# Optimization experiments

Hardware: AMD Instinct MI355X
Metric: run time of the kernel (lower is better)

## Reference

```python
import jax, jax.numpy as jnp
import numpy as np

BLOCK = 8      # block_size
HALO = 3       # halo_size
WIN = BLOCK + 2 * HALO   # 14, kv window size
NH = 8         # num_heads
DH = 32        # dim_head
DIM = 256
DIM_QK = NH * DH          # 256
DV = 256                  # dim_v = dim_out
DVH = DV // NH            # 32
SCALE = DH ** -0.5
REL = 2 * WIN - 1         # 27


def rel_logits_1d(q, rel_k, permute_mask):
    # q: (B, H, W, d); rel_k: (rel_size, d)
    B, H, W, d = q.shape
    rel_size = rel_k.shape[0]
    win = (rel_size + 1) // 2
    x = jnp.einsum('bhwd,rd->bhwr', q, rel_k).reshape(-1, W, rel_size)
    # skew trick: pad + reshape turns absolute into relative indexing
    x = jnp.pad(x, ((0, 0), (0, 0), (0, 1))).reshape(x.shape[0], -1)
    x = jnp.pad(x, ((0, 0), (0, rel_size - W))).reshape(-1, W + 1, rel_size)
    x = x[:, :W, win - 1:]
    x = jnp.broadcast_to(x.reshape(B, H, 1, W, win), (B, H, win, W, win))
    return jnp.transpose(x, permute_mask)


def pos_embed_rel(q, height_rel, width_rel):
    # q: (B*NH, num_blocks, block*block, DH)
    B, BB, HW, dh = q.shape
    q4 = q.reshape(-1, BLOCK, BLOCK, dh)
    rel_w = rel_logits_1d(q4, width_rel, (0, 1, 3, 2, 4))
    rel_h = rel_logits_1d(jnp.transpose(q4, (0, 2, 1, 3)), height_rel, (0, 3, 1, 4, 2))
    return (rel_h + rel_w).reshape(B, BB, HW, -1)


def setup_inputs() -> dict:
    key = jax.random.key(0)
    k1, k2, k3, k4, k5 = jax.random.split(key, 5)
    B, H, W = 4, 128, 128
    std = DIM ** -0.5
    return {
        'x': jax.random.normal(k1, (B, DIM, H, W), dtype=jnp.float32),
        'w_q': jax.random.normal(k2, (DIM_QK, DIM), dtype=jnp.float32) * std,
        'w_kv': jax.random.normal(k3, (DIM_QK + DV, DIM), dtype=jnp.float32) * std,
        'height_rel': jax.random.normal(k4, (REL, DH), dtype=jnp.float32) * SCALE,
        'width_rel': jax.random.normal(k5, (REL, DH), dtype=jnp.float32) * SCALE,
    }


def reference(x, w_q, w_kv, height_rel, width_rel):
    B, C, H, W = x.shape
    nhb, nwb = H // BLOCK, W // BLOCK
    nb = nhb * nwb
    # 1x1 convs as matmuls over channel dim
    q = jnp.einsum('bchw,oc->bohw', x, w_q)
    q = q.reshape(B * NH, DH, nhb, BLOCK, nwb, BLOCK)
    q = jnp.transpose(q, (0, 1, 3, 5, 2, 4)).reshape(B * NH, DH, BLOCK * BLOCK, nb)
    q = jnp.transpose(q, (0, 3, 2, 1))              # (B*NH, nb, bs^2, DH)

    kv = jnp.einsum('bchw,oc->bohw', x, w_kv)
    kv = jnp.pad(kv, ((0, 0), (0, 0), (HALO, HALO), (HALO, HALO)))
    ih = jnp.arange(nhb)[:, None] * BLOCK + jnp.arange(WIN)[None, :]
    iw = jnp.arange(nwb)[:, None] * BLOCK + jnp.arange(WIN)[None, :]
    kv = kv[:, :, ih]
    kv = kv[:, :, :, :, iw]
    kv = jnp.transpose(kv, (0, 1, 2, 4, 3, 5))
    kv = kv.reshape(B * NH, DH + DVH, nb, WIN * WIN)
    kv = jnp.transpose(kv, (0, 2, 3, 1))
    k, v = kv[..., :DH], kv[..., DH:]

    logits = jnp.einsum('bnqd,bnkd->bnqk', q, k) * SCALE
    logits = logits + pos_embed_rel(q, height_rel, width_rel)
    attn = jax.nn.softmax(logits, axis=-1)
    out = jnp.einsum('bnqk,bnkd->bnqd', attn, v)    # (B*NH, nb, bs^2, DVH)
    out = jnp.transpose(out, (0, 3, 2, 1))          # (B*NH, DVH, bs^2, nb)
    out = out.reshape(-1, BLOCK, BLOCK, nhb, nwb)
    out = jnp.transpose(out, (0, 3, 1, 4, 2)).reshape(B, DV, H, W)
    return out
```

## Files before the change

### kernel.cpp

```cpp
#include <hip/hip_runtime.h>
#include <stdint.h>


typedef short bf16s;
typedef bf16s bf16x8 __attribute__((ext_vector_type(8)));
typedef float f32x4  __attribute__((ext_vector_type(4)));
typedef unsigned int u32x4 __attribute__((ext_vector_type(4)));

#define MFMA16(a, b, c) __builtin_amdgcn_mfma_f32_16x16x32_bf16(a, b, c, 0, 0, 0)
#define SCALE_QK 0.17677669529663687f
#define LOG2E 1.4426950408889634f
#define EXP_SHIFT 11.541560327111707f

__device__ __forceinline__ void async16(void* lds, const void* g) {
  __builtin_amdgcn_global_load_lds(
      (const __attribute__((address_space(1))) unsigned int*)g,
      (__attribute__((address_space(3))) unsigned int*)lds, 16, 0, 0);
}

__device__ __forceinline__ bf16s f2b(float f) {
  unsigned int u = __builtin_bit_cast(unsigned int, f);
  u = (u + 0x7fffu + ((u >> 16) & 1u)) >> 16;
  return (bf16s)u;
}

__global__ __launch_bounds__(256) void k_convert(const float* __restrict__ wq,
                                                 const float* __restrict__ wkv,
                                                 const float* __restrict__ hrel,
                                                 const float* __restrict__ wrel,
                                                 bf16s* __restrict__ wq_b,
                                                 bf16s* __restrict__ wkv_b,
                                                 bf16s* __restrict__ rel_b) {
  int i = blockIdx.x * 256 + threadIdx.x;
  if (i < 65536) {
    wq_b[i] = f2b(wq[i]);
  } else if (i < 196608) {
    int j = i - 65536;
    wkv_b[j] = f2b(wkv[j]);
  } else {
    int r2 = i - 196608;
    int relid = r2 >> 10, r = (r2 >> 5) & 31, d = r2 & 31;
    const float* src = relid ? hrel : wrel;
    rel_b[r2] = (r < 27) ? f2b(src[r * 32 + d]) : (bf16s)0;
  }
}

__global__ __launch_bounds__(256) void k_transpose(const float* __restrict__ x,
                                                   bf16s* __restrict__ xT) {
  __shared__ bf16s tile[64][72];
  const int ct = blockIdx.x, pt = blockIdx.y, b = blockIdx.z;
  const int t = threadIdx.x;
  const int r0 = t >> 3, c8 = (t & 7) * 8;
  const float* src = x + ((size_t)b * 256 + ct * 64) * 16384 + (size_t)pt * 64;
#pragma unroll
  for (int pass = 0; pass < 2; ++pass) {
    int r = pass * 32 + r0;
    const float4* sp = (const float4*)(src + (size_t)r * 16384 + c8);
    float4 f0 = sp[0], f1 = sp[1];
    bf16x8 v;
    v[0] = f2b(f0.x); v[1] = f2b(f0.y); v[2] = f2b(f0.z); v[3] = f2b(f0.w);
    v[4] = f2b(f1.x); v[5] = f2b(f1.y); v[6] = f2b(f1.z); v[7] = f2b(f1.w);
    *(bf16x8*)&tile[r][c8] = v;
  }
  __syncthreads();
  bf16s* dst = xT + ((size_t)b * 16384 + pt * 64) * 256 + ct * 64;
#pragma unroll
  for (int pass = 0; pass < 2; ++pass) {
    int p = pass * 32 + r0;
    bf16x8 v;
#pragma unroll
    for (int u = 0; u < 8; ++u) v[u] = tile[c8 + u][p];
    *(bf16x8*)(dst + (size_t)p * 256 + c8) = v;
  }
}

__global__ __launch_bounds__(256) void k_zero_border(bf16s* __restrict__ kv) {
  const int gid = blockIdx.x * 256 + threadIdx.x;
  const int chunk = gid & 63;
  const int rest = gid >> 6;
  const int b = rest / 1572, pxi = rest % 1572;
  int y, x;
  if (pxi < 804) {
    int r = pxi / 134;
    x = pxi % 134;
    y = (r < 3) ? r : 128 + r;
  } else {
    int p2 = pxi - 804;
    y = 3 + p2 / 6;
    int xi = p2 % 6;
    x = (xi < 3) ? xi : 128 + xi;
  }
  u32x4 z = {0, 0, 0, 0};
  *(u32x4*)(kv + (((size_t)b * 134 + y) * 134 + x) * 512 + chunk * 8) = z;
}

__global__ __launch_bounds__(256) void k_qkv(const bf16s* __restrict__ wq,
                                             const bf16s* __restrict__ wkv,
                                             const bf16s* __restrict__ xT,
                                             bf16s* __restrict__ q_ws,
                                             bf16s* __restrict__ kv_ws) {
  __shared__ __align__(16) bf16s smem[17408];
  bf16s* Al = smem;
  bf16s* Bl = smem + 4096;
  const int mt = blockIdx.x, y = blockIdx.y, b = blockIdx.z;
  const int t = threadIdx.x;
  const int wv = t >> 6, lane = t & 63, g = lane >> 4, l15 = lane & 15;
  const int wm = wv & 1, wn = wv >> 1;
  const bf16s* Ag = (mt < 2) ? (wq + mt * 128 * 256) : (wkv + (mt - 2) * 128 * 256);
  const bf16s* Bg = xT + ((size_t)b * 16384 + y * 128) * 256;

  f32x4 acc[4][4];
#pragma unroll
  for (int i = 0; i < 4; ++i)
#pragma unroll
    for (int j = 0; j < 4; ++j) acc[i][j] = (f32x4){0.f, 0.f, 0.f, 0.f};

  for (int kc = 0; kc < 8; ++kc) {
    __syncthreads();
#pragma unroll
    for (int hh = 0; hh < 2; ++hh) {
      int tt = hh * 256 + t;
      int row = tt >> 2, k8 = (tt & 3) * 8;
      async16((char*)Al + hh * 4096 + wv * 1024, Ag + row * 256 + kc * 32 + k8);
      async16((char*)Bl + hh * 4096 + wv * 1024, Bg + row * 256 + kc * 32 + k8);
    }
    __syncthreads();
    bf16x8 af[4], bfr[4];
#pragma unroll
    for (int mi = 0; mi < 4; ++mi)
      af[mi] = *(const bf16x8*)&Al[(wm * 64 + mi * 16 + l15) * 32 + g * 8];
#pragma unroll
    for (int ni = 0; ni < 4; ++ni)
      bfr[ni] = *(const bf16x8*)&Bl[(wn * 64 + ni * 16 + l15) * 32 + g * 8];
#pragma unroll
    for (int mi = 0; mi < 4; ++mi)
#pragma unroll
      for (int ni = 0; ni < 4; ++ni)
        acc[mi][ni] = MFMA16(af[mi], bfr[ni], acc[mi][ni]);
  }

  __syncthreads();
  bf16s* Cl = smem;
#pragma unroll
  for (int mi = 0; mi < 4; ++mi)
#pragma unroll
    for (int ni = 0; ni < 4; ++ni)
#pragma unroll
      for (int rg = 0; rg < 4; ++rg) {
        int m = wm * 64 + mi * 16 + g * 4 + rg;
        int n = wn * 64 + ni * 16 + l15;
        Cl[n * 136 + m] = f2b(acc[mi][ni][rg]);
      }
  __syncthreads();

  if (mt < 2) {
#pragma unroll
    for (int hh = 0; hh < 2; ++hh) {
      int rid = hh * 256 + t;
      int head = rid >> 7, bx = (rid >> 3) & 15, wc = rid & 7;
      int px = bx * 8 + wc;
      bf16s* dst = q_ws +
          ((((size_t)(b * 8 + mt * 4 + head) * 256 + (y >> 3) * 16 + bx) * 64 +
            (y & 7) * 8 + wc)) * 32;
#pragma unroll
      for (int c4 = 0; c4 < 4; ++c4)
        *(bf16x8*)(dst + c4 * 8) = *(const bf16x8*)&Cl[px * 136 + head * 32 + c4 * 8];
    }
  } else {
    int px = t >> 1, half = t & 1;
    bf16s* dst = kv_ws + (((size_t)b * 134 + y + 3) * 134 + px + 3) * 512 +
                 (mt - 2) * 128 + half * 64;
#pragma unroll
    for (int c8 = 0; c8 < 8; ++c8)
      *(bf16x8*)(dst + c8 * 8) = *(const bf16x8*)&Cl[px * 136 + half * 64 + c8 * 8];
  }
}

__global__ __launch_bounds__(256, 3) void k_attn(const bf16s* __restrict__ q_ws,
                                                 const bf16s* __restrict__ kv_ws,
                                                 const bf16s* __restrict__ rel_b,
                                                 float* __restrict__ outp) {
  __shared__ __align__(16) char arena[43008];
  bf16s* vT = (bf16s*)arena;
  const int t = threadIdx.x;
  const int wv = t >> 6, lane = t & 63, g = lane >> 4, l15 = lane & 15;
  char* pw = arena + 14336 + wv * 7168;
  float* RWp = (float*)pw;
  float* RHp = RWp + 544;
  bf16s* pP  = (bf16s*)pw;

  int wgid = blockIdx.x;
  int xcd = wgid & 7, chnk = wgid >> 3;
  int bxlo = chnk & 3, rest = chnk >> 2;
  int c = xcd * 256 + rest;
  int bx = (c & 3) * 4 + bxlo;
  int byy = (c >> 2) & 15;
  int bh = c >> 6;
  int b = bh >> 3, hd = bh & 7;
  int blk = byy * 16 + bx;

  const bf16s* kvb = kv_ws + (((size_t)b * 134 + byy * 8) * 134 + bx * 8) * 512 + hd * 64;
  const bf16s* qg  = q_ws + ((size_t)bh * 256 + blk) * 2048;

  bf16x8 aq = *(const bf16x8*)(qg + (wv * 16 + l15) * 32 + g * 8);
  const int i_cl = (l15 < 14) ? l15 : 13;
  const bf16s* kbase = kvb + (size_t)i_cl * 68608 + g * 8;
  bf16x8 kf[14];
#pragma unroll
  for (int nt = 0; nt < 14; ++nt)
    kf[nt] = *(const bf16x8*)(kbase + nt * 512);
  bf16x8 wf[2], hf[2];
#pragma unroll
  for (int t16 = 0; t16 < 2; ++t16) {
    wf[t16] = *(const bf16x8*)(rel_b + (t16 * 16 + l15) * 32 + g * 8);
    hf[t16] = *(const bf16x8*)(rel_b + 1024 + (t16 * 16 + l15) * 32 + g * 8);
  }

  for (int idx = t; idx < 784; idx += 256) {
    int pos = idx >> 2, ch = idx & 3;
    int i = pos / 14, j = pos - i * 14;
    bf16x8 v = *(const bf16x8*)(kvb + (size_t)(i * 134 + j) * 512 + 32 + ch * 8);
#pragma unroll
    for (int u = 0; u < 8; ++u) vT[(ch * 8 + u) * 224 + j * 16 + i] = v[u];
  }
  for (int idx = t; idx < 896; idx += 256) {
    int d = idx / 28, r = idx - d * 28;
    vT[d * 224 + (r >> 1) * 16 + 14 + (r & 1)] = 0;
  }

  f32x4 acc[14];
#pragma unroll
  for (int nt = 0; nt < 14; ++nt) acc[nt] = (f32x4){0.f, 0.f, 0.f, 0.f};
#pragma unroll
  for (int nt = 0; nt < 14; ++nt) acc[nt] = MFMA16(kf[nt], aq, acc[nt]);

  {
    f32x4 zz = (f32x4){0.f, 0.f, 0.f, 0.f};
#pragma unroll
    for (int t16 = 0; t16 < 2; ++t16) {
      f32x4 rw = MFMA16(wf[t16], aq, zz);
      f32x4 rh = MFMA16(hf[t16], aq, zz);
#pragma unroll
      for (int rg = 0; rg < 4; ++rg) {
        RWp[l15 * 34 + t16 * 16 + g * 4 + rg] = rw[rg];
        RHp[l15 * 34 + t16 * 16 + g * 4 + rg] = rh[rg];
      }
    }
  }

  const int jq = l15 & 7;
  const int iq = wv * 2 + (l15 >> 3);
  const float* RWr = RWp + l15 * 34;
  const float* RHr = RHp + l15 * 34;
  const int ihb = 13 + g * 4 - iq;
  float h0 = RHr[ihb], h1 = RHr[ihb + 1], h2 = RHr[ihb + 2], h3 = RHr[ihb + 3];
  float sm = 0.f;
#pragma unroll
  for (int nt = 0; nt < 14; ++nt) {
    float w1 = RWr[13 + nt - jq];
    float e0 = exp2f(fmaf(fmaf(acc[nt][0], SCALE_QK, w1 + h0), LOG2E, -EXP_SHIFT));
    float e1 = exp2f(fmaf(fmaf(acc[nt][1], SCALE_QK, w1 + h1), LOG2E, -EXP_SHIFT));
    float e2 = exp2f(fmaf(fmaf(acc[nt][2], SCALE_QK, w1 + h2), LOG2E, -EXP_SHIFT));
    float e3 = exp2f(fmaf(fmaf(acc[nt][3], SCALE_QK, w1 + h3), LOG2E, -EXP_SHIFT));
    if (g == 3) { e2 = 0.f; e3 = 0.f; }
    sm += e0 + e1 + e2 + e3;
    acc[nt][0] = e0; acc[nt][1] = e1; acc[nt][2] = e2; acc[nt][3] = e3;
  }
  sm += __shfl_xor(sm, 16);
  sm += __shfl_xor(sm, 32);
  float rs = __builtin_amdgcn_rcpf(sm);

#pragma unroll
  for (int nt = 0; nt < 14; ++nt) {
    bf16s p0 = f2b(acc[nt][0] * rs), p1 = f2b(acc[nt][1] * rs);
    bf16s p2 = f2b(acc[nt][2] * rs), p3 = f2b(acc[nt][3] * rs);
    unsigned int lo = (unsigned short)p0 | ((unsigned int)(unsigned short)p1 << 16);
    unsigned int hi = (unsigned short)p2 | ((unsigned int)(unsigned short)p3 << 16);
    *(uint2*)(pP + l15 * 224 + nt * 16 + g * 4) = make_uint2(lo, hi);
  }

  __syncthreads();

  f32x4 oa0 = (f32x4){0.f, 0.f, 0.f, 0.f};
  f32x4 oa1 = (f32x4){0.f, 0.f, 0.f, 0.f};
#pragma unroll
  for (int ks = 0; ks < 7; ++ks) {
    bf16x8 bp = *(const bf16x8*)(pP + l15 * 224 + ks * 32 + g * 8);
    bf16x8 a0 = *(const bf16x8*)(vT + l15 * 224 + ks * 32 + g * 8);
    bf16x8 a1 = *(const bf16x8*)(vT + (16 + l15) * 224 + ks * 32 + g * 8);
    oa0 = MFMA16(a0, bp, oa0);
    oa1 = MFMA16(a1, bp, oa1);
  }

  {
    int py = wv * 2 + (l15 >> 3), px = l15 & 7;
    float* ob = outp + (((size_t)(b * 256 + hd * 32) * 128 + byy * 8 + py) * 128) +
                bx * 8 + px;
#pragma unroll
    for (int rg = 0; rg < 4; ++rg) {
      ob[(size_t)(g * 4 + rg) * 16384] = oa0[rg];
      ob[(size_t)(16 + g * 4 + rg) * 16384] = oa1[rg];
    }
  }
}

extern "C" void kernel_launch(void* const* d_in, const int* in_sizes, int n_in,
                              void* d_out, int out_size, void* d_ws, size_t ws_size,
                              hipStream_t stream) {
  (void)in_sizes; (void)n_in; (void)out_size; (void)ws_size;
  const float* x    = (const float*)d_in[0];
  const float* wq   = (const float*)d_in[1];
  const float* wkv  = (const float*)d_in[2];
  const float* hrel = (const float*)d_in[3];
  const float* wrel = (const float*)d_in[4];
  float* outp = (float*)d_out;

  bf16s* xT    = (bf16s*)d_ws;
  bf16s* q_ws  = xT + 16777216;
  bf16s* kv_ws = q_ws + 16777216;
  bf16s* wq_b  = kv_ws + 36773888;
  bf16s* wkv_b = wq_b + 65536;
  bf16s* rel_b = wkv_b + 131072;

  hipLaunchKernelGGL(k_convert,    dim3(776),       dim3(256), 0, stream,
                     wq, wkv, hrel, wrel, wq_b, wkv_b, rel_b);
  hipLaunchKernelGGL(k_transpose,  dim3(4, 256, 4), dim3(256), 0, stream, x, xT);
  hipLaunchKernelGGL(k_zero_border, dim3(1572),     dim3(256), 0, stream, kv_ws);
  hipLaunchKernelGGL(k_qkv,        dim3(6, 128, 4), dim3(256), 0, stream,
                     wq_b, wkv_b, xT, q_ws, kv_ws);
  hipLaunchKernelGGL(k_attn,       dim3(8192),      dim3(256), 0, stream,
                     q_ws, kv_ws, rel_b, outp);
}
```

Baseline: 300.8 us.

## Feed softmax probabilities to PV MFMA from registers, defer normalization

Drops the LDS round trip for the probability matrix. The exponentials stay in registers and feed 16x16x16 bf16 MFMAs directly, because that instruction's B-operand layout matches the accumulator layout of the QK product. Normalization by the row sum moves to the output store, and the log2e scale and shift are folded into the relative-position tables so the exponent takes one fma. The smaller LDS footprint allows launch bounds of 5 waves per SIMD, and the vT stride is padded to reduce bank conflicts; the risks are twice as many smaller MFMAs and more register pressure.

```diff
diff --git a/kernel.cpp b/kernel.cpp
--- a/kernel.cpp
+++ b/kernel.cpp
@@ -4,6 +4,7 @@
 
 typedef short bf16s;
 typedef bf16s bf16x8 __attribute__((ext_vector_type(8)));
+typedef bf16s bf16x4 __attribute__((ext_vector_type(4)));
 typedef float f32x4  __attribute__((ext_vector_type(4)));
 typedef unsigned int u32x4 __attribute__((ext_vector_type(4)));
 
@@ -11,6 +12,20 @@
 #define SCALE_QK 0.17677669529663687f
 #define LOG2E 1.4426950408889634f
 #define EXP_SHIFT 11.541560327111707f
+#define SCLOG 0.25503486142f
+
+__device__ __forceinline__ f32x4 pv_mfma(bf16x4 a, bf16x4 b, f32x4 c) {
+#if __has_builtin(__builtin_amdgcn_mfma_f32_16x16x16bf16_1k)
+  return __builtin_amdgcn_mfma_f32_16x16x16bf16_1k(a, b, c, 0, 0, 0);
+#elif __has_builtin(__builtin_amdgcn_mfma_f32_16x16x16_bf16)
+  return __builtin_amdgcn_mfma_f32_16x16x16_bf16(a, b, c, 0, 0, 0);
+#else
+  f32x4 d;
+  asm volatile("v_mfma_f32_16x16x16_bf16 %0, %1, %2, %3\n\ts_nop 4\n\ts_nop 4"
+               : "=v"(d) : "v"(a), "v"(b), "v"(c));
+  return d;
+#endif
+}
 
 __device__ __forceinline__ void async16(void* lds, const void* g) {
   __builtin_amdgcn_global_load_lds(
@@ -176,18 +191,18 @@
   }
 }
 
-__global__ __launch_bounds__(256, 3) void k_attn(const bf16s* __restrict__ q_ws,
+#define VSTRIDE 228
+__global__ __launch_bounds__(256, 5) void k_attn(const bf16s* __restrict__ q_ws,
                                                  const bf16s* __restrict__ kv_ws,
                                                  const bf16s* __restrict__ rel_b,
                                                  float* __restrict__ outp) {
-  __shared__ __align__(16) char arena[43008];
+  __shared__ __align__(16) char arena[32000];
   bf16s* vT = (bf16s*)arena;
   const int t = threadIdx.x;
   const int wv = t >> 6, lane = t & 63, g = lane >> 4, l15 = lane & 15;
-  char* pw = arena + 14336 + wv * 7168;
+  char* pw = arena + 14592 + wv * 4352;
   float* RWp = (float*)pw;
   float* RHp = RWp + 544;
-  bf16s* pP  = (bf16s*)pw;
 
   int wgid = blockIdx.x;
   int xcd = wgid & 7, chnk = wgid >> 3;
@@ -221,11 +236,11 @@
     int i = pos / 14, j = pos - i * 14;
     bf16x8 v = *(const bf16x8*)(kvb + (size_t)(i * 134 + j) * 512 + 32 + ch * 8);
 #pragma unroll
-    for (int u = 0; u < 8; ++u) vT[(ch * 8 + u) * 224 + j * 16 + i] = v[u];
+    for (int u = 0; u < 8; ++u) vT[(ch * 8 + u) * VSTRIDE + j * 16 + i] = v[u];
   }
   for (int idx = t; idx < 896; idx += 256) {
     int d = idx / 28, r = idx - d * 28;
-    vT[d * 224 + (r >> 1) * 16 + 14 + (r & 1)] = 0;
+    vT[d * VSTRIDE + (r >> 1) * 16 + 14 + (r & 1)] = 0;
   }
 
   f32x4 acc[14];
@@ -240,11 +255,14 @@
     for (int t16 = 0; t16 < 2; ++t16) {
       f32x4 rw = MFMA16(wf[t16], aq, zz);
       f32x4 rh = MFMA16(hf[t16], aq, zz);
-#pragma unroll
-      for (int rg = 0; rg < 4; ++rg) {
-        RWp[l15 * 34 + t16 * 16 + g * 4 + rg] = rw[rg];
-        RHp[l15 * 34 + t16 * 16 + g * 4 + rg] = rh[rg];
-      }
+      float* wd = &RWp[l15 * 34 + t16 * 16 + g * 4];
+      float* hd2 = &RHp[l15 * 34 + t16 * 16 + g * 4];
+      *(float2*)wd       = make_float2(fmaf(rw[0], LOG2E, -EXP_SHIFT),
+                                       fmaf(rw[1], LOG2E, -EXP_SHIFT));
+      *(float2*)(wd + 2) = make_float2(fmaf(rw[2], LOG2E, -EXP_SHIFT),
+                                       fmaf(rw[3], LOG2E, -EXP_SHIFT));
+      *(float2*)hd2       = make_float2(rh[0] * LOG2E, rh[1] * LOG2E);
+      *(float2*)(hd2 + 2) = make_float2(rh[2] * LOG2E, rh[3] * LOG2E);
     }
   }
 
@@ -258,10 +276,10 @@
 #pragma unroll
   for (int nt = 0; nt < 14; ++nt) {
     float w1 = RWr[13 + nt - jq];
-    float e0 = exp2f(fmaf(fmaf(acc[nt][0], SCALE_QK, w1 + h0), LOG2E, -EXP_SHIFT));
-    float e1 = exp2f(fmaf(fmaf(acc[nt][1], SCALE_QK, w1 + h1), LOG2E, -EXP_SHIFT));
-    float e2 = exp2f(fmaf(fmaf(acc[nt][2], SCALE_QK, w1 + h2), LOG2E, -EXP_SHIFT));
-    float e3 = exp2f(fmaf(fmaf(acc[nt][3], SCALE_QK, w1 + h3), LOG2E, -EXP_SHIFT));
+    float e0 = exp2f(fmaf(acc[nt][0], SCLOG, w1 + h0));
+    float e1 = exp2f(fmaf(acc[nt][1], SCLOG, w1 + h1));
+    float e2 = exp2f(fmaf(acc[nt][2], SCLOG, w1 + h2));
+    float e3 = exp2f(fmaf(acc[nt][3], SCLOG, w1 + h3));
     if (g == 3) { e2 = 0.f; e3 = 0.f; }
     sm += e0 + e1 + e2 + e3;
     acc[nt][0] = e0; acc[nt][1] = e1; acc[nt][2] = e2; acc[nt][3] = e3;
@@ -270,26 +288,19 @@
   sm += __shfl_xor(sm, 32);
   float rs = __builtin_amdgcn_rcpf(sm);
 
-#pragma unroll
-  for (int nt = 0; nt < 14; ++nt) {
-    bf16s p0 = f2b(acc[nt][0] * rs), p1 = f2b(acc[nt][1] * rs);
-    bf16s p2 = f2b(acc[nt][2] * rs), p3 = f2b(acc[nt][3] * rs);
-    unsigned int lo = (unsigned short)p0 | ((unsigned int)(unsigned short)p1 << 16);
-    unsigned int hi = (unsigned short)p2 | ((unsigned int)(unsigned short)p3 << 16);
-    *(uint2*)(pP + l15 * 224 + nt * 16 + g * 4) = make_uint2(lo, hi);
-  }
-
   __syncthreads();
 
   f32x4 oa0 = (f32x4){0.f, 0.f, 0.f, 0.f};
   f32x4 oa1 = (f32x4){0.f, 0.f, 0.f, 0.f};
 #pragma unroll
-  for (int ks = 0; ks < 7; ++ks) {
-    bf16x8 bp = *(const bf16x8*)(pP + l15 * 224 + ks * 32 + g * 8);
-    bf16x8 a0 = *(const bf16x8*)(vT + l15 * 224 + ks * 32 + g * 8);
-    bf16x8 a1 = *(const bf16x8*)(vT + (16 + l15) * 224 + ks * 32 + g * 8);
-    oa0 = MFMA16(a0, bp, oa0);
-    oa1 = MFMA16(a1, bp, oa1);
+  for (int nt = 0; nt < 14; ++nt) {
+    bf16x4 bpv;
+    bpv[0] = f2b(acc[nt][0]); bpv[1] = f2b(acc[nt][1]);
+    bpv[2] = f2b(acc[nt][2]); bpv[3] = f2b(acc[nt][3]);
+    bf16x4 a0 = *(const bf16x4*)(vT + l15 * VSTRIDE + nt * 16 + g * 4);
+    bf16x4 a1 = *(const bf16x4*)(vT + (16 + l15) * VSTRIDE + nt * 16 + g * 4);
+    oa0 = pv_mfma(a0, bpv, oa0);
+    oa1 = pv_mfma(a1, bpv, oa1);
   }
 
   {
@@ -298,8 +309,8 @@
                 bx * 8 + px;
 #pragma unroll
     for (int rg = 0; rg < 4; ++rg) {
-      ob[(size_t)(g * 4 + rg) * 16384] = oa0[rg];
-      ob[(size_t)(16 + g * 4 + rg) * 16384] = oa1[rg];
+      ob[(size_t)(g * 4 + rg) * 16384] = oa0[rg] * rs;
+      ob[(size_t)(16 + g * 4 + rg) * 16384] = oa1[rg] * rs;
     }
   }
 }
```

Result: faster. 281.7 us (-6.4%).
